# Performance work log

Measured on AMD Instinct MI355X. Metric: run time of the kernel, lower is better.

The kernel has to match this reference:

```python
import jax, jax.numpy as jnp
import numpy as np

B, S, V, E, H, L = 64, 512, 32000, 512, 512, 2


def setup_inputs() -> dict:
    key = jax.random.key(0)
    ks = jax.random.split(key, 8)
    x = jax.random.randint(ks[0], (B, S), 0, V, dtype=jnp.int64 if jax.config.jax_enable_x64 else jnp.int32)
    # pack_right_padded_seq assumes right-padded seqs; hidden[:ebs] slicing implies
    # lengths sorted in DESCENDING order. Enforce length >= 1.
    lengths = jnp.clip(jax.random.randint(ks[1], (B,), 0, S + 1), 1, S)
    lengths = jnp.sort(lengths)[::-1]
    scale = 1.0 / np.sqrt(H)
    emb = jax.random.normal(ks[2], (V, E), dtype=jnp.float32) * 0.02
    W_ih = jax.random.uniform(ks[3], (L, H, E), jnp.float32, -scale, scale)
    W_hh = jax.random.uniform(ks[4], (L, H, H), jnp.float32, -scale, scale)
    b_ih = jax.random.uniform(ks[5], (L, H), jnp.float32, -scale, scale)
    b_hh = jax.random.uniform(ks[6], (L, H), jnp.float32, -scale, scale)
    return {"x": x, "lengths": lengths, "emb": emb, "W_ih": W_ih,
            "W_hh": W_hh, "b_ih": b_ih, "b_hh": b_hh}


def reference(x, lengths, emb, W_ih, W_hh, b_ih, b_hh):
    # Equivalent to the packed-sequence loop: at timestep t, only sequences with
    # t < length are active (packing with descending lengths keeps them as the
    # leading rows). We express the same math with a mask + lax.scan.
    xe = jnp.swapaxes(emb[x], 0, 1)                       # [S, B, E]
    mask = jnp.arange(S)[:, None] < lengths[None, :]      # [S, B]
    h0 = jnp.zeros((B, L, H), dtype=emb.dtype)

    def step(h, inp):
        xt, m = inp                                        # [B,E], [B]
        cur = xt
        hs = []
        for l in range(L):
            hl = h[:, l]                                   # [B, H]
            hn = jnp.tanh(cur @ W_ih[l].T + b_ih[l] + hl @ W_hh[l].T + b_hh[l])
            hl = jnp.where(m[:, None], hn, hl)             # freeze finished seqs
            hs.append(hl)
            cur = hl                                       # next layer's input
        return jnp.stack(hs, axis=1), None

    hidden, _ = jax.lax.scan(step, h0, (xe, mask))
    out = hidden[:, -1]                                    # last layer final state
    return out, hidden
```

## Files before the change

kernel.cpp:

```cpp
#include <hip/hip_runtime.h>


#define BATCH 64
#define SEQ   512
#define HID   512
#define NTHR  256
#define CB    8
#define ROWS  32
#define SLOT  (BATCH * HID)
#define RING  8

typedef unsigned int u32;

__device__ __forceinline__ float dot4(const float4 a, const float4 b) {
  return a.x * b.x + a.y * b.y + a.z * b.z + a.w * b.w;
}
__device__ __forceinline__ float2 ld2(const double* p) {
  const double d = __hip_atomic_load(p, __ATOMIC_RELAXED, __HIP_MEMORY_SCOPE_AGENT);
  return __builtin_bit_cast(float2, d);
}
__device__ __forceinline__ void st2(double* p, float2 v) {
  __hip_atomic_store(p, __builtin_bit_cast(double, v),
                     __ATOMIC_RELAXED, __HIP_MEMORY_SCOPE_AGENT);
}
__device__ __forceinline__ float tanh_fast(float x) {
  const float a = fabsf(x);
  const float e = __expf(-2.0f * a);
  const float t = (1.0f - e) * __builtin_amdgcn_rcpf(1.0f + e);
  return copysignf(t, x);
}
#define WAIT_VM0() asm volatile("s_waitcnt vmcnt(0)" ::: "memory")

#define RSTEP(D, N)                                                   \
  {                                                                   \
    const bool hi = (lane & (D)) != 0;                                \
    _Pragma("unroll")                                                 \
    for (int a = 0; a < (N); ++a) {                                   \
      const float keep = hi ? v[a + (N)] : v[a];                      \
      const float send = hi ? v[a] : v[a + (N)];                      \
      v[a] = keep + __shfl_xor(send, (D));                            \
    }                                                                 \
  }

__global__ __launch_bounds__(NTHR, 1) void rnn_persistent(
    const int* __restrict__ x, const int* __restrict__ lengths,
    const float* __restrict__ emb,
    const float* __restrict__ W_ih, const float* __restrict__ W_hh,
    const float* __restrict__ b_ih, const float* __restrict__ b_hh,
    float* __restrict__ out,
    float* h0r, float* h1r, u32* F, int ring)
{
  __shared__ __align__(16) float Xa[CB][HID];
  __shared__ __align__(16) float Xb[CB][HID];
  __shared__ __align__(16) float Xpart[CB][ROWS][4];
  __shared__ int Lens[CB];

  const int wg    = blockIdx.x;
  const int tid   = threadIdx.x;
  const int dom   = wg & 7;
  const int q     = wg >> 3;
  const int layer = q >> 4;
  const int rg    = q & 15;
  const int bbase = dom * CB;
  const int jbase = rg * ROWS;
  const int tj    = tid >> 6;
  const int lane  = tid & 63;

  u32* Fown = F + ((dom * 2 + layer) * 16 + rg) * 32;
  u32* F0   = F + ((dom * 2 + 0) * 16) * 32;
  u32* F1   = F + ((dom * 2 + 1) * 16) * 32;

  float4 wa[2][8], wb[2][8];
  {
    const float* WA = W_ih + layer * (HID * HID);
    const float* WB = W_hh + layer * (HID * HID);
    #pragma unroll
    for (int ji = 0; ji < 8; ++ji) {
      const int j = jbase + tj * 8 + ji;
      #pragma unroll
      for (int i = 0; i < 2; ++i) {
        const int k = i * 256 + 4 * lane;
        wa[i][ji] = *(const float4*)&WA[j * HID + k];
        wb[i][ji] = *(const float4*)&WB[j * HID + k];
      }
    }
  }
  if (tid < CB) Lens[tid] = lengths[bbase + tid];
  __syncthreads();
  int maxlen = Lens[0];
  #pragma unroll
  for (int i = 1; i < CB; ++i) maxlen = max(maxlen, Lens[i]);
  const int P     = maxlen;
  const int pl0   = (P < SEQ) ? P : (SEQ - 1);
  const int plast = layer ? P : pl0;
  int lm[4];
  #pragma unroll
  for (int g = 0; g < 4; ++g) lm[g] = max(Lens[2 * g], Lens[2 * g + 1]);

  float4 bias4 = make_float4(0.f, 0.f, 0.f, 0.f);
  if (tid < 64) {
    const int jq = jbase + (tid & 7) * 4;
    bias4.x = b_ih[layer * HID + jq + 0] + b_hh[layer * HID + jq + 0];
    bias4.y = b_ih[layer * HID + jq + 1] + b_hh[layer * HID + jq + 1];
    bias4.z = b_ih[layer * HID + jq + 2] + b_hh[layer * HID + jq + 2];
    bias4.w = b_ih[layer * HID + jq + 3] + b_hh[layer * HID + jq + 3];
  }

  float4 pf[4];
  if (layer == 0) {
    #pragma unroll
    for (int i = 0; i < 4; ++i) {
      const int u = tid + NTHR * i;
      const int r = u >> 7, c = (u & 127) * 4;
      const int tok = x[(bbase + r) * SEQ];
      pf[i] = *(const float4*)&emb[(size_t)tok * HID + c];
    }
  }

  int cur = 0, prev = ring - 1;

  for (int p = 0; p <= P; ++p) {
    const bool active = layer ? (p >= 1) : (p < SEQ);
    const int  wr0    = (cur + 1 == ring) ? 0 : (cur + 1);

    if (active) {
      const int t = layer ? (p - 1) : p;

      if (layer == 0) {
        const double* src = (const double*)(h0r) + (size_t)cur * (SLOT / 2);
        float2 tv[8];
        #pragma unroll
        for (int i = 0; i < 8; ++i) {
          const int u = tid + NTHR * i;
          tv[i] = ld2(&src[(size_t)(bbase + (u >> 8)) * 256 + (u & 255)]);
        }
        #pragma unroll
        for (int i = 0; i < 8; ++i) {
          const int u = tid + NTHR * i;
          *(float2*)&Xb[u >> 8][(u & 255) * 2] = tv[i];
        }
        #pragma unroll
        for (int i = 0; i < 4; ++i) {
          const int u = tid + NTHR * i;
          *(float4*)&Xa[u >> 7][(u & 127) * 4] = pf[i];
        }
      } else {
        const double* srcB = (const double*)(h1r) + (size_t)prev * (SLOT / 2);
        const double* srcA = (const double*)(h0r) + (size_t)cur  * (SLOT / 2);
        float2 tb[8], ta[8];
        #pragma unroll
        for (int i = 0; i < 8; ++i) {
          const int u = tid + NTHR * i;
          tb[i] = ld2(&srcB[(size_t)(bbase + (u >> 8)) * 256 + (u & 255)]);
        }
        #pragma unroll
        for (int i = 0; i < 8; ++i) {
          const int u = tid + NTHR * i;
          ta[i] = ld2(&srcA[(size_t)(bbase + (u >> 8)) * 256 + (u & 255)]);
        }
        #pragma unroll
        for (int i = 0; i < 8; ++i) {
          const int u = tid + NTHR * i;
          *(float2*)&Xb[u >> 8][(u & 255) * 2] = tb[i];
          *(float2*)&Xa[u >> 8][(u & 255) * 2] = ta[i];
        }
      }
      __syncthreads();

      #pragma unroll 2
      for (int g = 0; g < 4; ++g) {
        if (t >= lm[g]) continue;
        float v[16];
        #pragma unroll
        for (int o = 0; o < 16; ++o) v[o] = 0.f;
        #pragma unroll
        for (int bi = 0; bi < 2; ++bi) {
          const int b = g * 2 + bi;
          const float4 xa0 = *(const float4*)&Xa[b][4 * lane];
          const float4 xa1 = *(const float4*)&Xa[b][256 + 4 * lane];
          const float4 xb0 = *(const float4*)&Xb[b][4 * lane];
          const float4 xb1 = *(const float4*)&Xb[b][256 + 4 * lane];
          #pragma unroll
          for (int ji = 0; ji < 8; ++ji) {
            v[bi * 8 + ji] += dot4(wa[0][ji], xa0) + dot4(wa[1][ji], xa1)
                            + dot4(wb[0][ji], xb0) + dot4(wb[1][ji], xb1);
          }
        }
        RSTEP(32, 8)
        RSTEP(16, 4)
        RSTEP(8, 2)
        RSTEP(4, 1)
        const int b_o = g * 2 + (lane >> 5);
        const int j_o = tj * 8 + ((lane >> 2) & 7);
        Xpart[b_o][j_o][lane & 3] = v[0];
      }
      __syncthreads();

      if (tid < 64) {
        const int b = tid >> 3, jq = (tid & 7) * 4;
        const float4 hb = *(const float4*)&Xb[b][jbase + jq];
        const bool live = (t < Lens[b]);
        float4 r = hb;
        if (live) {
          const float4 p0 = *(const float4*)&Xpart[b][jq + 0][0];
          const float4 p1 = *(const float4*)&Xpart[b][jq + 1][0];
          const float4 p2 = *(const float4*)&Xpart[b][jq + 2][0];
          const float4 p3 = *(const float4*)&Xpart[b][jq + 3][0];
          r.x = tanh_fast(p0.x + p0.y + p0.z + p0.w + bias4.x);
          r.y = tanh_fast(p1.x + p1.y + p1.z + p1.w + bias4.y);
          r.z = tanh_fast(p2.x + p2.y + p2.z + p2.w + bias4.z);
          r.w = tanh_fast(p3.x + p3.y + p3.z + p3.w + bias4.w);
        }
        double* dst = layer ? ((double*)h1r + (size_t)cur * (SLOT / 2))
                            : ((double*)h0r + (size_t)wr0 * (SLOT / 2));
        const size_t di = (size_t)(bbase + b) * 256 + ((jbase + jq) >> 1);
        st2(&dst[di],     make_float2(r.x, r.y));
        st2(&dst[di + 1], make_float2(r.z, r.w));
        if (p == plast) {
          if (layer == 0) {
            *(float4*)&out[32768 + (size_t)(bbase + b) * 1024 + jbase + jq] = r;
          } else {
            *(float4*)&out[(size_t)(bbase + b) * 512 + jbase + jq] = r;
            *(float4*)&out[32768 + (size_t)(bbase + b) * 1024 + 512 + jbase + jq] = r;
          }
        }
      }
    }

    WAIT_VM0();
    if (tid == 0 && active)
      __hip_atomic_store(Fown, (u32)(layer ? p : (p + 1)),
                         __ATOMIC_RELAXED, __HIP_MEMORY_SCOPE_AGENT);
    __syncthreads();
    const int np = p + 1;
    if (layer == 0 && np <= plast) {
      #pragma unroll
      for (int i = 0; i < 4; ++i) {
        const int u = tid + NTHR * i;
        const int r = u >> 7, c = (u & 127) * 4;
        const int tok = x[(bbase + r) * SEQ + np];
        pf[i] = *(const float4*)&emb[(size_t)tok * HID + c];
      }
    }
    if (np <= P) {
      if (tid < 64) {
        u32* fp  = Fown;
        u32  tgt = 0;
        bool ok  = true;
        if (lane < 16) { fp = F0 + lane * 32; tgt = (u32)np; ok = false; }
        else if (lane < 32) {
          if (layer) { fp = F1 + (lane - 16) * 32; tgt = (u32)(np - 1); ok = false; }
          else {
            const int th = np + 1 - ring;
            if (th > 0) { fp = F1 + (lane - 16) * 32; tgt = (u32)th; ok = false; }
          }
        }
        while (true) {
          if (!ok) ok = (__hip_atomic_load(fp, __ATOMIC_RELAXED,
                                           __HIP_MEMORY_SCOPE_AGENT) >= tgt);
          if (__ballot(ok) == ~0ull) break;
          __builtin_amdgcn_s_sleep(1);
        }
      }
      __syncthreads();
    }
    prev = cur; cur = wr0;
  }
}

extern "C" void kernel_launch(void* const* d_in, const int* in_sizes, int n_in,
                              void* d_out, int out_size, void* d_ws, size_t ws_size,
                              hipStream_t stream) {
  (void)in_sizes; (void)n_in; (void)out_size; (void)ws_size;
  const int*   x       = (const int*)d_in[0];
  const int*   lengths = (const int*)d_in[1];
  const float* emb     = (const float*)d_in[2];
  const float* W_ih    = (const float*)d_in[3];
  const float* W_hh    = (const float*)d_in[4];
  const float* b_ih    = (const float*)d_in[5];
  const float* b_hh    = (const float*)d_in[6];
  float* out = (float*)d_out;

  const size_t slotB = (size_t)SLOT * sizeof(float);
  const int ring = RING;

  float* h0r = (float*)d_ws;
  float* h1r = h0r + (size_t)ring * SLOT;
  u32*   F   = (u32*)(h1r + (size_t)ring * SLOT);

  hipMemsetAsync(h0r, 0, slotB, stream);
  hipMemsetAsync(h1r, 0, slotB, stream);
  hipMemsetAsync(F, 0, 32768, stream);

  hipLaunchKernelGGL(rnn_persistent, dim3(256), dim3(NTHR), 0, stream,
                     x, lengths, emb, W_ih, W_hh, b_ih, b_hh, out,
                     h0r, h1r, F, ring);
}
```

Measured before the change: 2.952 ms.

## Split RNN step into input and recurrent phases to overlap flag waits with compute

Each timestep now computes the input-projection half of the matvec (W_ih times the layer input) first. Only after that does it wait on the recurrent-state flags and load h_{t-1} for the W_hh half, so the input contribution is computed while the wave would otherwise be spinning. The flag wait moves from the end of the step into the step itself, with separate waits for layer 1's input dependency and for the recurrent dependency, and the flag publish is done by the writer threads right after their stores. Every thread now runs its own ballot spin loop, and ordering across workgroups rests on relaxed atomics plus vmcnt waits, which risks extra polling traffic or subtle ordering issues.

```diff
diff --git a/kernel.cpp b/kernel.cpp
--- a/kernel.cpp
+++ b/kernel.cpp
@@ -22,6 +22,9 @@
 __device__ __forceinline__ void st2(double* p, float2 v) {
   __hip_atomic_store(p, __builtin_bit_cast(double, v),
                      __ATOMIC_RELAXED, __HIP_MEMORY_SCOPE_AGENT);
+}
+__device__ __forceinline__ u32 ldf(const u32* p) {
+  return __hip_atomic_load(p, __ATOMIC_RELAXED, __HIP_MEMORY_SCOPE_AGENT);
 }
 __device__ __forceinline__ float tanh_fast(float x) {
   const float a = fabsf(x);
@@ -126,28 +129,87 @@
     if (active) {
       const int t = layer ? (p - 1) : p;
 
+      if (layer) {
+        const u32* fp = F0 + (lane & 15) * 32;
+        bool ok = (lane >= 16);
+        while (true) {
+          if (!ok) ok = (ldf(fp) >= (u32)p);
+          if (__ballot(ok) == ~0ull) break;
+          __builtin_amdgcn_s_sleep(1);
+        }
+      }
+
       if (layer == 0) {
-        const double* src = (const double*)(h0r) + (size_t)cur * (SLOT / 2);
-        float2 tv[8];
+        #pragma unroll
+        for (int i = 0; i < 4; ++i) {
+          const int u = tid + NTHR * i;
+          *(float4*)&Xa[u >> 7][(u & 127) * 4] = pf[i];
+        }
+      } else {
+        const double* srcA = (const double*)(h0r) + (size_t)cur * (SLOT / 2);
+        float2 ta[8];
         #pragma unroll
         for (int i = 0; i < 8; ++i) {
           const int u = tid + NTHR * i;
-          tv[i] = ld2(&src[(size_t)(bbase + (u >> 8)) * 256 + (u & 255)]);
+          ta[i] = ld2(&srcA[(size_t)(bbase + (u >> 8)) * 256 + (u & 255)]);
         }
         #pragma unroll
         for (int i = 0; i < 8; ++i) {
           const int u = tid + NTHR * i;
-          *(float2*)&Xb[u >> 8][(u & 255) * 2] = tv[i];
-        }
-        #pragma unroll
-        for (int i = 0; i < 4; ++i) {
-          const int u = tid + NTHR * i;
-          *(float4*)&Xa[u >> 7][(u & 127) * 4] = pf[i];
-        }
-      } else {
-        const double* srcB = (const double*)(h1r) + (size_t)prev * (SLOT / 2);
-        const double* srcA = (const double*)(h0r) + (size_t)cur  * (SLOT / 2);
-        float2 tb[8], ta[8];
+          *(float2*)&Xa[u >> 8][(u & 255) * 2] = ta[i];
+        }
+      }
+      __syncthreads();
+
+      float va1[4];
+      #pragma unroll
+      for (int g = 0; g < 4; ++g) {
+        va1[g] = 0.f;
+        if (t >= lm[g]) continue;
+        float v[16];
+        #pragma unroll
+        for (int o = 0; o < 16; ++o) v[o] = 0.f;
+        #pragma unroll
+        for (int bi = 0; bi < 2; ++bi) {
+          const int b = g * 2 + bi;
+          const float4 xa0 = *(const float4*)&Xa[b][4 * lane];
+          const float4 xa1 = *(const float4*)&Xa[b][256 + 4 * lane];
+          #pragma unroll
+          for (int ji = 0; ji < 8; ++ji) {
+            v[bi * 8 + ji] += dot4(wa[0][ji], xa0) + dot4(wa[1][ji], xa1);
+          }
+        }
+        RSTEP(32, 8)
+        RSTEP(16, 4)
+        RSTEP(8, 2)
+        RSTEP(4, 1)
+        va1[g] = v[0];
+      }
+
+      {
+        const u32* fp = Fown;
+        u32 tgt = 0;
+        bool ok = true;
+        if (lane < 16) {
+          fp = (layer ? F1 : F0) + lane * 32;
+          tgt = layer ? (u32)(p - 1) : (u32)p;
+          ok = false;
+        } else if (lane < 32 && layer == 0) {
+          const int th = p + 1 - ring;
+          if (th > 0) { fp = F1 + (lane - 16) * 32; tgt = (u32)th; ok = false; }
+        }
+        while (true) {
+          if (!ok) ok = (ldf(fp) >= tgt);
+          if (__ballot(ok) == ~0ull) break;
+          __builtin_amdgcn_s_sleep(1);
+        }
+      }
+
+      {
+        const double* srcB = layer
+            ? (const double*)(h1r) + (size_t)prev * (SLOT / 2)
+            : (const double*)(h0r) + (size_t)cur  * (SLOT / 2);
+        float2 tb[8];
         #pragma unroll
         for (int i = 0; i < 8; ++i) {
           const int u = tid + NTHR * i;
@@ -156,13 +218,7 @@
         #pragma unroll
         for (int i = 0; i < 8; ++i) {
           const int u = tid + NTHR * i;
-          ta[i] = ld2(&srcA[(size_t)(bbase + (u >> 8)) * 256 + (u & 255)]);
-        }
-        #pragma unroll
-        for (int i = 0; i < 8; ++i) {
-          const int u = tid + NTHR * i;
           *(float2*)&Xb[u >> 8][(u & 255) * 2] = tb[i];
-          *(float2*)&Xa[u >> 8][(u & 255) * 2] = ta[i];
         }
       }
       __syncthreads();
@@ -176,14 +232,11 @@
         #pragma unroll
         for (int bi = 0; bi < 2; ++bi) {
           const int b = g * 2 + bi;
-          const float4 xa0 = *(const float4*)&Xa[b][4 * lane];
-          const float4 xa1 = *(const float4*)&Xa[b][256 + 4 * lane];
           const float4 xb0 = *(const float4*)&Xb[b][4 * lane];
           const float4 xb1 = *(const float4*)&Xb[b][256 + 4 * lane];
           #pragma unroll
           for (int ji = 0; ji < 8; ++ji) {
-            v[bi * 8 + ji] += dot4(wa[0][ji], xa0) + dot4(wa[1][ji], xa1)
-                            + dot4(wb[0][ji], xb0) + dot4(wb[1][ji], xb1);
+            v[bi * 8 + ji] += dot4(wb[0][ji], xb0) + dot4(wb[1][ji], xb1);
           }
         }
         RSTEP(32, 8)
@@ -192,7 +245,7 @@
         RSTEP(4, 1)
         const int b_o = g * 2 + (lane >> 5);
         const int j_o = tj * 8 + ((lane >> 2) & 7);
-        Xpart[b_o][j_o][lane & 3] = v[0];
+        Xpart[b_o][j_o][lane & 3] = v[0] + va1[g];
       }
       __syncthreads();
 
@@ -224,14 +277,13 @@
             *(float4*)&out[32768 + (size_t)(bbase + b) * 1024 + 512 + jbase + jq] = r;
           }
         }
+        WAIT_VM0();
+        if (tid == 0)
+          __hip_atomic_store(Fown, (u32)(layer ? p : (p + 1)),
+                             __ATOMIC_RELAXED, __HIP_MEMORY_SCOPE_AGENT);
       }
     }
 
-    WAIT_VM0();
-    if (tid == 0 && active)
-      __hip_atomic_store(Fown, (u32)(layer ? p : (p + 1)),
-                         __ATOMIC_RELAXED, __HIP_MEMORY_SCOPE_AGENT);
-    __syncthreads();
     const int np = p + 1;
     if (layer == 0 && np <= plast) {
       #pragma unroll
@@ -241,28 +293,6 @@
         const int tok = x[(bbase + r) * SEQ + np];
         pf[i] = *(const float4*)&emb[(size_t)tok * HID + c];
       }
-    }
-    if (np <= P) {
-      if (tid < 64) {
-        u32* fp  = Fown;
-        u32  tgt = 0;
-        bool ok  = true;
-        if (lane < 16) { fp = F0 + lane * 32; tgt = (u32)np; ok = false; }
-        else if (lane < 32) {
-          if (layer) { fp = F1 + (lane - 16) * 32; tgt = (u32)(np - 1); ok = false; }
-          else {
-            const int th = np + 1 - ring;
-            if (th > 0) { fp = F1 + (lane - 16) * 32; tgt = (u32)th; ok = false; }
-          }
-        }
-        while (true) {
-          if (!ok) ok = (__hip_atomic_load(fp, __ATOMIC_RELAXED,
-                                           __HIP_MEMORY_SCOPE_AGENT) >= tgt);
-          if (__ballot(ok) == ~0ull) break;
-          __builtin_amdgcn_s_sleep(1);
-        }
-      }
-      __syncthreads();
     }
     prev = cur; cur = wr0;
   }
```

After: 3.750 ms. 1.27x slower.

## Halve workgroup count, doubling rows and threads per persistent workgroup

Applied to the files above, without the earlier changes.

The persistent RNN kernel now runs 128 workgroups of 512 threads, each owning 64 hidden rows instead of 32. The staging loops, bias setup, epilogue and flag-wait lanes are resized to match. Each step then has fewer flags to poll and fewer workgroups to synchronize, and the global reloads of h per row are cut in half. In exchange each workgroup does more work per step, and half as many CUs are in use.

```diff
diff --git a/kernel.cpp b/kernel.cpp
--- a/kernel.cpp
+++ b/kernel.cpp
@@ -4,9 +4,10 @@
 #define BATCH 64
 #define SEQ   512
 #define HID   512
-#define NTHR  256
+#define NTHR  512
 #define CB    8
-#define ROWS  32
+#define ROWS  64
+#define NWG   8
 #define SLOT  (BATCH * HID)
 #define RING  8
 
@@ -22,6 +23,9 @@
 __device__ __forceinline__ void st2(double* p, float2 v) {
   __hip_atomic_store(p, __builtin_bit_cast(double, v),
                      __ATOMIC_RELAXED, __HIP_MEMORY_SCOPE_AGENT);
+}
+__device__ __forceinline__ u32 ldf(const u32* p) {
+  return __hip_atomic_load(p, __ATOMIC_RELAXED, __HIP_MEMORY_SCOPE_AGENT);
 }
 __device__ __forceinline__ float tanh_fast(float x) {
   const float a = fabsf(x);
@@ -59,16 +63,16 @@
   const int tid   = threadIdx.x;
   const int dom   = wg & 7;
   const int q     = wg >> 3;
-  const int layer = q >> 4;
-  const int rg    = q & 15;
+  const int layer = q >> 3;
+  const int rg    = q & 7;
   const int bbase = dom * CB;
   const int jbase = rg * ROWS;
   const int tj    = tid >> 6;
   const int lane  = tid & 63;
 
-  u32* Fown = F + ((dom * 2 + layer) * 16 + rg) * 32;
-  u32* F0   = F + ((dom * 2 + 0) * 16) * 32;
-  u32* F1   = F + ((dom * 2 + 1) * 16) * 32;
+  u32* Fown = F + ((dom * 2 + layer) * NWG + rg) * 32;
+  u32* F0   = F + ((dom * 2 + 0) * NWG) * 32;
+  u32* F1   = F + ((dom * 2 + 1) * NWG) * 32;
 
   float4 wa[2][8], wb[2][8];
   {
@@ -97,19 +101,24 @@
   #pragma unroll
   for (int g = 0; g < 4; ++g) lm[g] = max(Lens[2 * g], Lens[2 * g + 1]);
 
-  float4 bias4 = make_float4(0.f, 0.f, 0.f, 0.f);
+  float4 bias4[2] = {make_float4(0.f, 0.f, 0.f, 0.f),
+                     make_float4(0.f, 0.f, 0.f, 0.f)};
   if (tid < 64) {
-    const int jq = jbase + (tid & 7) * 4;
-    bias4.x = b_ih[layer * HID + jq + 0] + b_hh[layer * HID + jq + 0];
-    bias4.y = b_ih[layer * HID + jq + 1] + b_hh[layer * HID + jq + 1];
-    bias4.z = b_ih[layer * HID + jq + 2] + b_hh[layer * HID + jq + 2];
-    bias4.w = b_ih[layer * HID + jq + 3] + b_hh[layer * HID + jq + 3];
-  }
-
-  float4 pf[4];
+    #pragma unroll
+    for (int k = 0; k < 2; ++k) {
+      const int idx = tid + 64 * k;
+      const int jq = jbase + (idx & 15) * 4;
+      bias4[k].x = b_ih[layer * HID + jq + 0] + b_hh[layer * HID + jq + 0];
+      bias4[k].y = b_ih[layer * HID + jq + 1] + b_hh[layer * HID + jq + 1];
+      bias4[k].z = b_ih[layer * HID + jq + 2] + b_hh[layer * HID + jq + 2];
+      bias4[k].w = b_ih[layer * HID + jq + 3] + b_hh[layer * HID + jq + 3];
+    }
+  }
+
+  float4 pf[2];
   if (layer == 0) {
     #pragma unroll
-    for (int i = 0; i < 4; ++i) {
+    for (int i = 0; i < 2; ++i) {
       const int u = tid + NTHR * i;
       const int r = u >> 7, c = (u & 127) * 4;
       const int tok = x[(bbase + r) * SEQ];
@@ -128,38 +137,38 @@
 
       if (layer == 0) {
         const double* src = (const double*)(h0r) + (size_t)cur * (SLOT / 2);
-        float2 tv[8];
-        #pragma unroll
-        for (int i = 0; i < 8; ++i) {
+        float2 tv[4];
+        #pragma unroll
+        for (int i = 0; i < 4; ++i) {
           const int u = tid + NTHR * i;
           tv[i] = ld2(&src[(size_t)(bbase + (u >> 8)) * 256 + (u & 255)]);
         }
         #pragma unroll
-        for (int i = 0; i < 8; ++i) {
+        for (int i = 0; i < 4; ++i) {
           const int u = tid + NTHR * i;
           *(float2*)&Xb[u >> 8][(u & 255) * 2] = tv[i];
         }
         #pragma unroll
-        for (int i = 0; i < 4; ++i) {
+        for (int i = 0; i < 2; ++i) {
           const int u = tid + NTHR * i;
           *(float4*)&Xa[u >> 7][(u & 127) * 4] = pf[i];
         }
       } else {
         const double* srcB = (const double*)(h1r) + (size_t)prev * (SLOT / 2);
         const double* srcA = (const double*)(h0r) + (size_t)cur  * (SLOT / 2);
-        float2 tb[8], ta[8];
-        #pragma unroll
-        for (int i = 0; i < 8; ++i) {
+        float2 tb[4], ta[4];
+        #pragma unroll
+        for (int i = 0; i < 4; ++i) {
           const int u = tid + NTHR * i;
           tb[i] = ld2(&srcB[(size_t)(bbase + (u >> 8)) * 256 + (u & 255)]);
         }
         #pragma unroll
-        for (int i = 0; i < 8; ++i) {
+        for (int i = 0; i < 4; ++i) {
           const int u = tid + NTHR * i;
           ta[i] = ld2(&srcA[(size_t)(bbase + (u >> 8)) * 256 + (u & 255)]);
         }
         #pragma unroll
-        for (int i = 0; i < 8; ++i) {
+        for (int i = 0; i < 4; ++i) {
           const int u = tid + NTHR * i;
           *(float2*)&Xb[u >> 8][(u & 255) * 2] = tb[i];
           *(float2*)&Xa[u >> 8][(u & 255) * 2] = ta[i];
@@ -197,31 +206,35 @@
       __syncthreads();
 
       if (tid < 64) {
-        const int b = tid >> 3, jq = (tid & 7) * 4;
-        const float4 hb = *(const float4*)&Xb[b][jbase + jq];
-        const bool live = (t < Lens[b]);
-        float4 r = hb;
-        if (live) {
-          const float4 p0 = *(const float4*)&Xpart[b][jq + 0][0];
-          const float4 p1 = *(const float4*)&Xpart[b][jq + 1][0];
-          const float4 p2 = *(const float4*)&Xpart[b][jq + 2][0];
-          const float4 p3 = *(const float4*)&Xpart[b][jq + 3][0];
-          r.x = tanh_fast(p0.x + p0.y + p0.z + p0.w + bias4.x);
-          r.y = tanh_fast(p1.x + p1.y + p1.z + p1.w + bias4.y);
-          r.z = tanh_fast(p2.x + p2.y + p2.z + p2.w + bias4.z);
-          r.w = tanh_fast(p3.x + p3.y + p3.z + p3.w + bias4.w);
-        }
-        double* dst = layer ? ((double*)h1r + (size_t)cur * (SLOT / 2))
-                            : ((double*)h0r + (size_t)wr0 * (SLOT / 2));
-        const size_t di = (size_t)(bbase + b) * 256 + ((jbase + jq) >> 1);
-        st2(&dst[di],     make_float2(r.x, r.y));
-        st2(&dst[di + 1], make_float2(r.z, r.w));
-        if (p == plast) {
-          if (layer == 0) {
-            *(float4*)&out[32768 + (size_t)(bbase + b) * 1024 + jbase + jq] = r;
-          } else {
-            *(float4*)&out[(size_t)(bbase + b) * 512 + jbase + jq] = r;
-            *(float4*)&out[32768 + (size_t)(bbase + b) * 1024 + 512 + jbase + jq] = r;
+        #pragma unroll
+        for (int k = 0; k < 2; ++k) {
+          const int idx = tid + 64 * k;
+          const int b = idx >> 4, jq = (idx & 15) * 4;
+          const float4 hb = *(const float4*)&Xb[b][jbase + jq];
+          const bool live = (t < Lens[b]);
+          float4 r = hb;
+          if (live) {
+            const float4 p0 = *(const float4*)&Xpart[b][jq + 0][0];
+            const float4 p1 = *(const float4*)&Xpart[b][jq + 1][0];
+            const float4 p2 = *(const float4*)&Xpart[b][jq + 2][0];
+            const float4 p3 = *(const float4*)&Xpart[b][jq + 3][0];
+            r.x = tanh_fast(p0.x + p0.y + p0.z + p0.w + bias4[k].x);
+            r.y = tanh_fast(p1.x + p1.y + p1.z + p1.w + bias4[k].y);
+            r.z = tanh_fast(p2.x + p2.y + p2.z + p2.w + bias4[k].z);
+            r.w = tanh_fast(p3.x + p3.y + p3.z + p3.w + bias4[k].w);
+          }
+          double* dst = layer ? ((double*)h1r + (size_t)cur * (SLOT / 2))
+                              : ((double*)h0r + (size_t)wr0 * (SLOT / 2));
+          const size_t di = (size_t)(bbase + b) * 256 + ((jbase + jq) >> 1);
+          st2(&dst[di],     make_float2(r.x, r.y));
+          st2(&dst[di + 1], make_float2(r.z, r.w));
+          if (p == plast) {
+            if (layer == 0) {
+              *(float4*)&out[32768 + (size_t)(bbase + b) * 1024 + jbase + jq] = r;
+            } else {
+              *(float4*)&out[(size_t)(bbase + b) * 512 + jbase + jq] = r;
+              *(float4*)&out[32768 + (size_t)(bbase + b) * 1024 + 512 + jbase + jq] = r;
+            }
           }
         }
       }
@@ -235,7 +248,7 @@
     const int np = p + 1;
     if (layer == 0 && np <= plast) {
       #pragma unroll
-      for (int i = 0; i < 4; ++i) {
+      for (int i = 0; i < 2; ++i) {
         const int u = tid + NTHR * i;
         const int r = u >> 7, c = (u & 127) * 4;
         const int tok = x[(bbase + r) * SEQ + np];
@@ -247,17 +260,17 @@
         u32* fp  = Fown;
         u32  tgt = 0;
         bool ok  = true;
-        if (lane < 16) { fp = F0 + lane * 32; tgt = (u32)np; ok = false; }
-        else if (lane < 32) {
-          if (layer) { fp = F1 + (lane - 16) * 32; tgt = (u32)(np - 1); ok = false; }
-          else {
+        if (lane < NWG) { fp = F0 + lane * 32; tgt = (u32)np; ok = false; }
+        else if (lane < 2 * NWG) {
+          if (layer) {
+            fp = F1 + (lane - NWG) * 32; tgt = (u32)(np - 1); ok = false;
+          } else {
             const int th = np + 1 - ring;
-            if (th > 0) { fp = F1 + (lane - 16) * 32; tgt = (u32)th; ok = false; }
+            if (th > 0) { fp = F1 + (lane - NWG) * 32; tgt = (u32)th; ok = false; }
           }
         }
         while (true) {
-          if (!ok) ok = (__hip_atomic_load(fp, __ATOMIC_RELAXED,
-                                           __HIP_MEMORY_SCOPE_AGENT) >= tgt);
+          if (!ok) ok = (ldf(fp) >= tgt);
           if (__ballot(ok) == ~0ull) break;
           __builtin_amdgcn_s_sleep(1);
         }
@@ -292,7 +305,7 @@
   hipMemsetAsync(h1r, 0, slotB, stream);
   hipMemsetAsync(F, 0, 32768, stream);
 
-  hipLaunchKernelGGL(rnn_persistent, dim3(256), dim3(NTHR), 0, stream,
+  hipLaunchKernelGGL(rnn_persistent, dim3(128), dim3(NTHR), 0, stream,
                      x, lengths, emb, W_ih, W_hh, b_ih, b_hh, out,
                      h0r, h1r, F, ring);
 }
```

Result: slower. 3.650 ms (+23.6%).
